# Kernel tuning notes

Measured on AMD Instinct MI355X. Metric: run time of the kernel, lower is better.

The kernel has to match this reference:

```python
import jax, jax.numpy as jnp
import numpy as np

INP_DIM, EMB_DIM, NUM_HEADS = 2048, 512, 2
LAMBDA_ATTN = 10.0
BS, L = 16, 1024


def _l2norm(x, axis=-1, eps=1e-12):
    # matches torch F.normalize: x / max(||x||, eps)
    n = jnp.sqrt(jnp.sum(x * x, axis=axis, keepdims=True))
    return x / jnp.maximum(n, eps)


def setup_inputs() -> dict:
    key = jax.random.key(0)
    k1, k2, kw, kb = jax.random.split(key, 4)
    img1 = jax.random.normal(k1, (BS, INP_DIM, L), dtype=jnp.float32)
    img2 = jax.random.normal(k2, (BS, INP_DIM, L), dtype=jnp.float32)
    # per-head query projection weights, stacked: (H, inp_dim, emb_dim)
    lim = 1.0 / np.sqrt(INP_DIM)
    W = jax.random.uniform(kw, (NUM_HEADS, INP_DIM, EMB_DIM), jnp.float32, -lim, lim)
    b = jax.random.uniform(kb, (NUM_HEADS, EMB_DIM), jnp.float32, -lim, lim)
    return {"img1": img1, "img2": img2, "W": W, "b": b}


def reference(img1, img2, W, b):
    # img1, img2: (bs, inp_dim, L) -> (bs, L, inp_dim)
    x1 = jnp.swapaxes(img1, 1, 2)
    x2 = jnp.swapaxes(img2, 1, 2)
    # per-head query projections: (H, bs, L, emb)
    q1 = jnp.einsum('bld,hde->hble', x1, W) + b[:, None, None, :]
    q2 = jnp.einsum('bld,hde->hble', x2, W) + b[:, None, None, :]
    # cosine relevance (attn_normalized=True): (H, bs, L, L)
    n1 = _l2norm(q1)
    n2 = _l2norm(q2)
    rel = jnp.einsum('hble,hbme->hblm', n1, n2) * LAMBDA_ATTN
    row_attn = jax.nn.softmax(rel, axis=3)  # softmax over img2 positions (dim=2 in torch)
    col_attn = jax.nn.softmax(rel, axis=2)  # softmax over img1 positions (dim=1 in torch)
    sim12 = row_attn.sum(axis=2)  # (H, bs, L) -> weight on img2 positions
    sim21 = col_attn.sum(axis=3)  # (H, bs, L) -> weight on img1 positions
    sim12 = sim12 / (sim12.sum(axis=-1, keepdims=True) + 1e-8)
    sim21 = sim21 / (sim21.sum(axis=-1, keepdims=True) + 1e-8)
    # torch module returns lists sim_in_img1 (=sim21) and sim_in_img2 (=sim12);
    # stack them: (2, H, bs, L)
    return jnp.stack([sim21, sim12], axis=0)
```

## Files before the change

kernel.cpp:

```cpp
#include <hip/hip_runtime.h>
#include <cstdint>
#include <cstddef>

#define INP 2048
#define EMB 512
#define NHEAD 2
#define BSZ 16
#define SEQ 1024
#define LAMBDA 10.0f

typedef __attribute__((ext_vector_type(8))) short bf16x8;
typedef __attribute__((ext_vector_type(16))) float f32x16;

__device__ __forceinline__ short f2bf(float x) {
    union { float f; unsigned u; } v; v.f = x;
    unsigned r = v.u + 0x7fffu + ((v.u >> 16) & 1u);
    return (short)(r >> 16);
}
__device__ __forceinline__ float bf2f(short h) {
    union { unsigned u; float f; } v; v.u = ((unsigned)(unsigned short)h) << 16;
    return v.f;
}
__device__ __forceinline__ void g2lds16(const void* g, void* l) {
    __builtin_amdgcn_global_load_lds(
        (const __attribute__((address_space(1))) unsigned int*)g,
        (__attribute__((address_space(3))) unsigned int*)l, 16, 0, 0);
}

__global__ __launch_bounds__(256) void zero_kernel(float* __restrict__ p, int n) {
    int i = blockIdx.x * 256 + threadIdx.x;
    if (i < n) p[i] = 0.f;
}

__global__ __launch_bounds__(256) void conv_t(const float* __restrict__ src,
                                              short* __restrict__ hi, int L) {
    const int l0 = blockIdx.x * 64;
    const int d0 = blockIdx.y * 32;
    const float* s = src + (size_t)blockIdx.z * INP * L;

    __shared__ float tl[32][65];
    const int t  = threadIdx.x;
    const int dr = t >> 3;
    const int f4 = (t & 7) * 4;

    float4 v0 = *(const float4*)&s[(size_t)(d0 + dr) * L + l0 + f4];
    float4 v1 = *(const float4*)&s[(size_t)(d0 + dr) * L + l0 + f4 + 32];
    tl[dr][f4 + 0] = v0.x; tl[dr][f4 + 1] = v0.y; tl[dr][f4 + 2] = v0.z; tl[dr][f4 + 3] = v0.w;
    tl[dr][f4 + 32] = v1.x; tl[dr][f4 + 33] = v1.y; tl[dr][f4 + 34] = v1.z; tl[dr][f4 + 35] = v1.w;
    __syncthreads();

    const int kgl = t >> 6;
    const int l   = t & 63;
    bf16x8 hv8;
#pragma unroll
    for (int q = 0; q < 8; q++) hv8[q] = f2bf(tl[kgl * 8 + q][l]);
    const size_t slot = (size_t)blockIdx.z * (INP / 8) * L
                      + (size_t)(blockIdx.y * 4 + kgl) * L + l0 + l;
    *(bf16x8*)&hi[slot * 8] = hv8;
}

__global__ __launch_bounds__(512, 2) void proj_gemm(
    const short* __restrict__ iT, const short* __restrict__ Wt,
    const float* __restrict__ bias, float* __restrict__ Q) {
    const int bid = blockIdx.x;
    const int xcd = bid & 7;
    const int s   = bid >> 3;
    const int g   = s >> 2;
    const int v   = s & 3;
    const int h   = v >> 1;
    const int nh  = v & 1;
    const int gg  = xcd * 16 + g;
    const int slab  = gg >> 2;
    const int mtile = gg & 3;
    const int mb = mtile * 256;
    const int nb = nh * 256;
    const int im = slab >> 4;
    const int b  = slab & 15;
    const int z  = (im * 2 + h) * 16 + b;

    const short* __restrict__ Ag = iT + (size_t)slab * (INP / 8) * SEQ * 8;
    const short* __restrict__ Bg = Wt + (size_t)h * (INP / 8) * EMB * 8;

    __shared__ short sL[4][16384];

    const int tid  = threadIdx.x;
    const int lane = tid & 63;
    const int wid  = tid >> 6;
    const int wm   = (wid >> 2) * 128;
    const int wn   = (wid & 3) * 64;
    const int fm   = lane & 31;
    const int khl  = lane >> 5;

    const int sgp = wid >> 2;
    const int srq = wid & 3;

    float bj[2];
#pragma unroll
    for (int j = 0; j < 2; j++) bj[j] = bias[h * EMB + nb + wn + j * 32 + fm];
    asm volatile("s_waitcnt vmcnt(0)" ::: "memory");

#define STAGE(tt) { \
    const int k8_ = (tt) * 4; \
    short* bA_ = &sL[(tt) & 3][0]; \
    short* bB_ = &sL[(tt) & 3][8192]; \
    g2lds16(Ag + ((size_t)(k8_ + sgp) * SEQ + mb + srq * 64 + lane) * 8, \
            bA_ + (sgp * 256 + srq * 64) * 8); \
    g2lds16(Ag + ((size_t)(k8_ + sgp + 2) * SEQ + mb + srq * 64 + lane) * 8, \
            bA_ + ((sgp + 2) * 256 + srq * 64) * 8); \
    g2lds16(Bg + ((size_t)(k8_ + sgp) * EMB + nb + srq * 64 + lane) * 8, \
            bB_ + (sgp * 256 + srq * 64) * 8); \
    g2lds16(Bg + ((size_t)(k8_ + sgp + 2) * EMB + nb + srq * 64 + lane) * 8, \
            bB_ + ((sgp + 2) * 256 + srq * 64) * 8); \
}

    f32x16 acc[4][2];
#pragma unroll
    for (int i = 0; i < 4; i++)
#pragma unroll
        for (int j = 0; j < 2; j++)
#pragma unroll
            for (int r = 0; r < 16; r++) acc[i][j][r] = 0.f;

    STAGE(0);
    STAGE(1);
    asm volatile("s_waitcnt vmcnt(4)" ::: "memory");
    __builtin_amdgcn_s_barrier();

    for (int t = 0; t < 64; t++) {
        if (t < 62) STAGE(t + 2);

        const short* bA = &sL[t & 3][0];
        const short* bB = &sL[t & 3][8192];
        bf16x8 af[4][2], bf[2][2];
#pragma unroll
        for (int ks = 0; ks < 2; ks++) {
            const int pl = (ks * 2 + khl) * 256;
#pragma unroll
            for (int i = 0; i < 4; i++)
                af[i][ks] = *(const bf16x8*)&bA[(pl + wm + i * 32 + fm) * 8];
#pragma unroll
            for (int j = 0; j < 2; j++)
                bf[j][ks] = *(const bf16x8*)&bB[(pl + wn + j * 32 + fm) * 8];
        }
        __builtin_amdgcn_s_setprio(1);
#pragma unroll
        for (int ks = 0; ks < 2; ks++)
#pragma unroll
            for (int i = 0; i < 4; i++)
#pragma unroll
                for (int j = 0; j < 2; j++)
                    acc[i][j] = __builtin_amdgcn_mfma_f32_32x32x16_bf16(af[i][ks], bf[j][ks], acc[i][j], 0, 0, 0);
        __builtin_amdgcn_s_setprio(0);

        if (t < 62)       asm volatile("s_waitcnt vmcnt(4)" ::: "memory");
        else if (t == 62) asm volatile("s_waitcnt vmcnt(0)" ::: "memory");
        if (t < 63) __builtin_amdgcn_s_barrier();
    }
#undef STAGE

    float* __restrict__ Qz = Q + (size_t)z * SEQ * EMB;
#pragma unroll
    for (int i = 0; i < 4; i++)
#pragma unroll
        for (int r = 0; r < 16; r++) {
            const int row = mb + wm + i * 32 + (r & 3) + 8 * (r >> 2) + khl * 4;
#pragma unroll
            for (int j = 0; j < 2; j++)
                Qz[(size_t)row * EMB + nb + wn + j * 32 + fm] = acc[i][j][r] + bj[j];
        }
}

__global__ __launch_bounds__(256) void norm_split(const float* __restrict__ Q,
                                                  short* __restrict__ Qhi) {
    const int z  = blockIdx.y;
    const int r0 = blockIdx.x * 4;
    const int t  = threadIdx.x;
    const int w    = t >> 6;
    const int lane = t & 63;
    const float* p = Q + ((size_t)z * SEQ + r0 + w) * EMB;

    float4 a = *(const float4*)&p[lane * 8];
    float4 b = *(const float4*)&p[lane * 8 + 4];
    float sq = a.x * a.x + a.y * a.y + a.z * a.z + a.w * a.w
             + b.x * b.x + b.y * b.y + b.z * b.z + b.w * b.w;
#pragma unroll
    for (int o = 32; o > 0; o >>= 1) sq += __shfl_xor(sq, o);
    float scale = 1.f / fmaxf(sqrtf(sq), 1e-12f);
    if (z < NHEAD * BSZ) scale *= LAMBDA;

    float v[8] = {a.x * scale, a.y * scale, a.z * scale, a.w * scale,
                  b.x * scale, b.y * scale, b.z * scale, b.w * scale};
    bf16x8 hv8;
#pragma unroll
    for (int q = 0; q < 8; q++) hv8[q] = f2bf(v[q]);
    __shared__ short shi[64 * 4 * 8];
    *(bf16x8*)&shi[(lane * 4 + w) * 8] = hv8;
    __syncthreads();

    const int kg = t >> 2, rl = t & 3;
    const size_t dst = ((size_t)z * (EMB / 8) + kg) * SEQ + r0 + rl;
    *(bf16x8*)&Qhi[dst * 8] = *(const bf16x8*)&shi[t * 8];
}

__global__ __launch_bounds__(256) void attn_mfma(
    const short* __restrict__ Qhi,
    short* __restrict__ E, float* __restrict__ Zr, float* __restrict__ Zc) {
    const int bid = blockIdx.x;
    const int xcd = bid & 7;
    const int s   = bid >> 3;
    const int hb  = xcd * 4 + (s >> 6);
    const int t   = s & 63;
    const int lt  = t & 7;
    const int mt  = t >> 3;
    const int l0 = lt * 128;
    const int m0 = mt * 128;

    const short* __restrict__ Ah = Qhi + (size_t)hb * SEQ * EMB;
    const short* __restrict__ Bh = Qhi + (size_t)(NHEAD * BSZ + hb) * SEQ * EMB;

    __shared__ short sA[4096], sB[4096];
    __shared__ float redR[128], redC[128];

    const int tid  = threadIdx.x;
    const int lane = tid & 63;
    const int wid  = tid >> 6;
    const int wm = (wid & 1) * 64;
    const int wn = (wid >> 1) * 64;
    const int fm = lane & 31;
    const int khl = lane >> 5;

    const short* gB = (wid & 2) ? Bh : Ah;
    short* lB = (wid & 2) ? sB : sA;
    const int rb = (wid & 2) ? m0 : l0;
    const int gb = (wid & 1) * 2;

    f32x16 acc[2][2];
#pragma unroll
    for (int i = 0; i < 2; i++)
#pragma unroll
        for (int j = 0; j < 2; j++)
#pragma unroll
            for (int r = 0; r < 16; r++) acc[i][j][r] = 0.f;

    for (int k0 = 0; k0 < EMB; k0 += 32) {
        const int k08 = k0 >> 3;
        __syncthreads();
#pragma unroll
        for (int v = 0; v < 4; v++) {
            const int g = gb + (v >> 1), hh = v & 1;
            g2lds16(gB + ((size_t)(k08 + g) * SEQ + rb + hh * 64 + lane) * 8,
                    lB + (g * 128 + hh * 64) * 8);
        }
        __syncthreads();

        bf16x8 afh[2][2], bfh[2][2];
#pragma unroll
        for (int i = 0; i < 2; i++)
#pragma unroll
            for (int ks = 0; ks < 2; ks++) {
                const int ra = ((ks * 2 + khl) * 128 + wm + i * 32 + fm) * 8;
                afh[i][ks] = *(const bf16x8*)&sA[ra];
                const int rbi = ((ks * 2 + khl) * 128 + wn + i * 32 + fm) * 8;
                bfh[i][ks] = *(const bf16x8*)&sB[rbi];
            }
#pragma unroll
        for (int ks = 0; ks < 2; ks++)
#pragma unroll
            for (int i = 0; i < 2; i++)
#pragma unroll
                for (int j = 0; j < 2; j++)
                    acc[i][j] = __builtin_amdgcn_mfma_f32_32x32x16_bf16(afh[i][ks], bfh[j][ks], acc[i][j], 0, 0, 0);
    }

    if (tid < 128) { redR[tid] = 0.f; redC[tid] = 0.f; }
    __syncthreads();

    short* __restrict__ Ez = E + (size_t)hb * SEQ * SEQ;
    const int rhalf = khl * 4;
    float cj0 = 0.f, cj1 = 0.f;
#pragma unroll
    for (int i = 0; i < 2; i++)
#pragma unroll
        for (int r = 0; r < 16; r++) {
            const int row = wm + i * 32 + (r & 3) + 8 * (r >> 2) + rhalf;
            const short e0s = f2bf(expf(acc[i][0][r]));
            const short e1s = f2bf(expf(acc[i][1][r]));
            const float e0v = bf2f(e0s);
            const float e1v = bf2f(e1s);
            Ez[(size_t)(l0 + row) * SEQ + m0 + wn + fm]      = e0s;
            Ez[(size_t)(l0 + row) * SEQ + m0 + wn + 32 + fm] = e1s;
            float rv = e0v + e1v;
#pragma unroll
            for (int o = 16; o > 0; o >>= 1) rv += __shfl_xor(rv, o);
            if ((lane & 31) == 0) atomicAdd(&redR[row], rv);
            cj0 += e0v; cj1 += e1v;
        }
    cj0 += __shfl_xor(cj0, 32);
    cj1 += __shfl_xor(cj1, 32);
    if (lane < 32) {
        atomicAdd(&redC[wn + fm], cj0);
        atomicAdd(&redC[wn + 32 + fm], cj1);
    }
    __syncthreads();

    if (tid < 128) {
        atomicAdd(&Zr[hb * SEQ + l0 + tid], redR[tid]);
        atomicAdd(&Zc[hb * SEQ + m0 + tid], redC[tid]);
    }
}

__global__ __launch_bounds__(256) void reduce_pass(
    const short* __restrict__ E, const float* __restrict__ Zr,
    const float* __restrict__ Zc, float* __restrict__ S21, float* __restrict__ S12) {
    const int lblk = blockIdx.x;
    const int hb   = blockIdx.y;
    const int tid  = threadIdx.x;
    const int lane = tid & 63;
    const int wid  = tid >> 6;
    const short* __restrict__ Ez = E + (size_t)hb * SEQ * SEQ;

    __shared__ float colred[SEQ];
    for (int i = tid; i < SEQ; i += 256) colred[i] = 0.f;
    __syncthreads();

    float izc[2][8];
#pragma unroll
    for (int it = 0; it < 2; it++)
#pragma unroll
        for (int q = 0; q < 8; q++)
            izc[it][q] = 1.f / Zc[hb * SEQ + it * 512 + lane * 8 + q];

    float colacc[2][8];
#pragma unroll
    for (int it = 0; it < 2; it++)
#pragma unroll
        for (int q = 0; q < 8; q++) colacc[it][q] = 0.f;

    for (int rr = 0; rr < 32; rr++) {
        const int row = lblk * 128 + wid * 32 + rr;
        const float izr = 1.f / Zr[hb * SEQ + row];
        float rowsum = 0.f;
#pragma unroll
        for (int it = 0; it < 2; it++) {
            bf16x8 ev = *(const bf16x8*)&Ez[(size_t)row * SEQ + it * 512 + lane * 8];
#pragma unroll
            for (int q = 0; q < 8; q++) {
                const float e = bf2f(ev[q]);
                rowsum += e * izc[it][q];
                colacc[it][q] += e * izr;
            }
        }
#pragma unroll
        for (int o = 32; o > 0; o >>= 1) rowsum += __shfl_down(rowsum, o);
        if (lane == 0) S21[hb * SEQ + row] = rowsum;
    }
#pragma unroll
    for (int it = 0; it < 2; it++)
#pragma unroll
        for (int q = 0; q < 8; q++)
            atomicAdd(&colred[it * 512 + lane * 8 + q], colacc[it][q]);
    __syncthreads();
    for (int i = tid; i < SEQ; i += 256) atomicAdd(&S12[hb * SEQ + i], colred[i]);
}

__global__ __launch_bounds__(256) void fin_kernel(
    const float* __restrict__ S21, const float* __restrict__ S12,
    float* __restrict__ out) {
    const int z  = blockIdx.x;
    const int w  = z / (NHEAD * BSZ);
    const int hb = z % (NHEAD * BSZ);
    const float* __restrict__ src = (w == 0 ? S21 : S12) + (size_t)hb * SEQ;
    const int t = threadIdx.x;

    float s = 0.f;
    for (int i = t; i < SEQ; i += 256) s += src[i];
#pragma unroll
    for (int o = 32; o > 0; o >>= 1) s += __shfl_down(s, o);
    __shared__ float red[4];
    if ((t & 63) == 0) red[t >> 6] = s;
    __syncthreads();
    const float total = red[0] + red[1] + red[2] + red[3];
    const float inv = 1.f / (total + 1e-8f);
    for (int i = t; i < SEQ; i += 256)
        out[(size_t)z * SEQ + i] = src[i] * inv;
}

extern "C" void kernel_launch(void* const* d_in, const int* in_sizes, int n_in,
                              void* d_out, int out_size, void* d_ws, size_t ws_size,
                              hipStream_t stream) {
    const float* img1 = (const float*)d_in[0];
    const float* img2 = (const float*)d_in[1];
    const float* W    = (const float*)d_in[2];
    const float* bias = (const float*)d_in[3];
    float* out = (float*)d_out;

    const size_t QN  = (size_t)2 * NHEAD * BSZ * SEQ * EMB;
    const size_t WN  = (size_t)NHEAD * EMB * INP;
    const size_t CNF = (size_t)32 * SEQ * INP;

    short* Qhi = (short*)d_ws;
    short* Wth = Qhi + QN;
    short* iTh = Wth + WN;
    float* Q   = (float*)(iTh + CNF);
    short* E   = (short*)Q;
    float* Zr  = Q + QN;
    float* Zc  = Zr + (size_t)NHEAD * BSZ * SEQ;
    float* S21 = Zc + (size_t)NHEAD * BSZ * SEQ;
    float* S12 = S21 + (size_t)NHEAD * BSZ * SEQ;

    zero_kernel<<<dim3(512), dim3(256), 0, stream>>>(Zr, 4 * NHEAD * BSZ * SEQ);

    conv_t<<<dim3(EMB / 64, INP / 32, NHEAD), dim3(256), 0, stream>>>(W, Wth, EMB);

    conv_t<<<dim3(SEQ / 64, INP / 32, 16), dim3(256), 0, stream>>>(img1, iTh, SEQ);
    conv_t<<<dim3(SEQ / 64, INP / 32, 16), dim3(256), 0, stream>>>(
        img2, iTh + (size_t)16 * (INP / 8) * SEQ * 8, SEQ);

    proj_gemm<<<dim3(512), dim3(512), 0, stream>>>(iTh, Wth, bias, Q);

    norm_split<<<dim3(SEQ / 4, 2 * NHEAD * BSZ), dim3(256), 0, stream>>>(Q, Qhi);

    attn_mfma<<<dim3(2048), dim3(256), 0, stream>>>(Qhi, E, Zr, Zc);

    reduce_pass<<<dim3(8, NHEAD * BSZ), dim3(256), 0, stream>>>(E, Zr, Zc, S21, S12);

    fin_kernel<<<dim3(2 * NHEAD * BSZ), dim3(256), 0, stream>>>(S21, S12, out);
    (void)in_sizes; (void)n_in; (void)out_size; (void)ws_size;
}
```

Before: 555.8 us.

## Switch projection and attention GEMMs to FP8 MFMA with register double-buffering

```diff
diff --git a/kernel.cpp b/kernel.cpp
--- a/kernel.cpp
+++ b/kernel.cpp
@@ -26,6 +26,40 @@
         (const __attribute__((address_space(1))) unsigned int*)g,
         (__attribute__((address_space(3))) unsigned int*)l, 16, 0, 0);
 }
+template <bool HI>
+__device__ __forceinline__ int pk8(float a, float b, int old) {
+    return __builtin_amdgcn_cvt_pk_fp8_f32(a, b, old, HI);
+}
+__device__ __forceinline__ void pack8f8(const float* v, unsigned* lo, unsigned* hi) {
+    int l = pk8<false>(v[0], v[1], 0); l = pk8<true>(v[2], v[3], l);
+    int h = pk8<false>(v[4], v[5], 0); h = pk8<true>(v[6], v[7], h);
+    *lo = (unsigned)l; *hi = (unsigned)h;
+}
+
+#define VM2() asm volatile("s_waitcnt vmcnt(2)" ::: "memory")
+#define VM0() asm volatile("s_waitcnt vmcnt(0)" ::: "memory")
+
+#define MFMAS(AO, BO) do { \
+    __builtin_amdgcn_s_setprio(1); \
+    _Pragma("unroll") for (int ks_ = 0; ks_ < 2; ks_++) \
+    _Pragma("unroll") for (int i_ = 0; i_ < 4; i_++) \
+    _Pragma("unroll") for (int j_ = 0; j_ < 2; j_++) \
+        acc[i_][j_] = __builtin_amdgcn_mfma_f32_32x32x16_fp8_fp8( \
+            AO[i_][ks_], BO[j_][ks_], acc[i_][j_], 0, 0, 0); \
+    __builtin_amdgcn_s_setprio(0); \
+} while (0)
+
+#define READF(AO, BO, sl) do { \
+    const char* bA_ = &sL[(sl)][0]; \
+    const char* bB_ = &sL[(sl)][8192]; \
+    _Pragma("unroll") for (int ks_ = 0; ks_ < 2; ks_++) { \
+        const int pl_ = (ks_ * 2 + khl) * 256; \
+        _Pragma("unroll") for (int i_ = 0; i_ < 4; i_++) \
+            AO[i_][ks_] = *(const long*)&bA_[(pl_ + wm + i_ * 32 + fm) * 8]; \
+        _Pragma("unroll") for (int j_ = 0; j_ < 2; j_++) \
+            BO[j_][ks_] = *(const long*)&bB_[(pl_ + wn + j_ * 32 + fm) * 8]; \
+    } \
+} while (0)
 
 __global__ __launch_bounds__(256) void zero_kernel(float* __restrict__ p, int n) {
     int i = blockIdx.x * 256 + threadIdx.x;
@@ -33,7 +67,7 @@
 }
 
 __global__ __launch_bounds__(256) void conv_t(const float* __restrict__ src,
-                                              short* __restrict__ hi, int L) {
+                                              char* __restrict__ out, int L) {
     const int l0 = blockIdx.x * 64;
     const int d0 = blockIdx.y * 32;
     const float* s = src + (size_t)blockIdx.z * INP * L;
@@ -51,16 +85,19 @@
 
     const int kgl = t >> 6;
     const int l   = t & 63;
-    bf16x8 hv8;
-#pragma unroll
-    for (int q = 0; q < 8; q++) hv8[q] = f2bf(tl[kgl * 8 + q][l]);
+    float v[8];
+#pragma unroll
+    for (int q = 0; q < 8; q++) v[q] = tl[kgl * 8 + q][l];
+    uint2 w;
+    pack8f8(v, &w.x, &w.y);
+
     const size_t slot = (size_t)blockIdx.z * (INP / 8) * L
                       + (size_t)(blockIdx.y * 4 + kgl) * L + l0 + l;
-    *(bf16x8*)&hi[slot * 8] = hv8;
+    *(uint2*)&out[slot * 8] = w;
 }
 
 __global__ __launch_bounds__(512, 2) void proj_gemm(
-    const short* __restrict__ iT, const short* __restrict__ Wt,
+    const char* __restrict__ iT, const char* __restrict__ Wt,
     const float* __restrict__ bias, float* __restrict__ Q) {
     const int bid = blockIdx.x;
     const int xcd = bid & 7;
@@ -78,10 +115,10 @@
     const int b  = slab & 15;
     const int z  = (im * 2 + h) * 16 + b;
 
-    const short* __restrict__ Ag = iT + (size_t)slab * (INP / 8) * SEQ * 8;
-    const short* __restrict__ Bg = Wt + (size_t)h * (INP / 8) * EMB * 8;
-
-    __shared__ short sL[4][16384];
+    const char* __restrict__ Ag = iT + (size_t)slab * INP * SEQ;
+    const char* __restrict__ Bg = Wt + (size_t)h * INP * EMB;
+
+    __shared__ char sL[4][16384];
 
     const int tid  = threadIdx.x;
     const int lane = tid & 63;
@@ -91,27 +128,18 @@
     const int fm   = lane & 31;
     const int khl  = lane >> 5;
 
-    const int sgp = wid >> 2;
-    const int srq = wid & 3;
+#define P_STAGE(tt) do { \
+    const int k8_ = (tt) * 4 + (wid >> 1); \
+    const int ro_ = (wid & 1) * 128 + lane * 2; \
+    char* d_ = &sL[(tt) & 3][(wid >> 1) * 2048 + (wid & 1) * 1024 + lane * 16]; \
+    g2lds16(Ag + ((size_t)k8_ * SEQ + mb + ro_) * 8, d_); \
+    g2lds16(Bg + ((size_t)k8_ * EMB + nb + ro_) * 8, d_ + 8192); \
+} while (0)
 
     float bj[2];
 #pragma unroll
     for (int j = 0; j < 2; j++) bj[j] = bias[h * EMB + nb + wn + j * 32 + fm];
-    asm volatile("s_waitcnt vmcnt(0)" ::: "memory");
-
-#define STAGE(tt) { \
-    const int k8_ = (tt) * 4; \
-    short* bA_ = &sL[(tt) & 3][0]; \
-    short* bB_ = &sL[(tt) & 3][8192]; \
-    g2lds16(Ag + ((size_t)(k8_ + sgp) * SEQ + mb + srq * 64 + lane) * 8, \
-            bA_ + (sgp * 256 + srq * 64) * 8); \
-    g2lds16(Ag + ((size_t)(k8_ + sgp + 2) * SEQ + mb + srq * 64 + lane) * 8, \
-            bA_ + ((sgp + 2) * 256 + srq * 64) * 8); \
-    g2lds16(Bg + ((size_t)(k8_ + sgp) * EMB + nb + srq * 64 + lane) * 8, \
-            bB_ + (sgp * 256 + srq * 64) * 8); \
-    g2lds16(Bg + ((size_t)(k8_ + sgp + 2) * EMB + nb + srq * 64 + lane) * 8, \
-            bB_ + ((sgp + 2) * 256 + srq * 64) * 8); \
-}
+    VM0();
 
     f32x16 acc[4][2];
 #pragma unroll
@@ -121,42 +149,28 @@
 #pragma unroll
             for (int r = 0; r < 16; r++) acc[i][j][r] = 0.f;
 
-    STAGE(0);
-    STAGE(1);
-    asm volatile("s_waitcnt vmcnt(4)" ::: "memory");
+    long a0[4][2], b0[2][2], a1[4][2], b1[2][2];
+
+    P_STAGE(0); P_STAGE(1); P_STAGE(2);
+    VM2();
     __builtin_amdgcn_s_barrier();
-
-    for (int t = 0; t < 64; t++) {
-        if (t < 62) STAGE(t + 2);
-
-        const short* bA = &sL[t & 3][0];
-        const short* bB = &sL[t & 3][8192];
-        bf16x8 af[4][2], bf[2][2];
-#pragma unroll
-        for (int ks = 0; ks < 2; ks++) {
-            const int pl = (ks * 2 + khl) * 256;
-#pragma unroll
-            for (int i = 0; i < 4; i++)
-                af[i][ks] = *(const bf16x8*)&bA[(pl + wm + i * 32 + fm) * 8];
-#pragma unroll
-            for (int j = 0; j < 2; j++)
-                bf[j][ks] = *(const bf16x8*)&bB[(pl + wn + j * 32 + fm) * 8];
-        }
-        __builtin_amdgcn_s_setprio(1);
-#pragma unroll
-        for (int ks = 0; ks < 2; ks++)
-#pragma unroll
-            for (int i = 0; i < 4; i++)
-#pragma unroll
-                for (int j = 0; j < 2; j++)
-                    acc[i][j] = __builtin_amdgcn_mfma_f32_32x32x16_bf16(af[i][ks], bf[j][ks], acc[i][j], 0, 0, 0);
-        __builtin_amdgcn_s_setprio(0);
-
-        if (t < 62)       asm volatile("s_waitcnt vmcnt(4)" ::: "memory");
-        else if (t == 62) asm volatile("s_waitcnt vmcnt(0)" ::: "memory");
-        if (t < 63) __builtin_amdgcn_s_barrier();
-    }
-#undef STAGE
+    READF(a0, b0, 0);
+
+    for (int t = 0; t < 64; t += 2) {
+        if (t + 3 < 64) P_STAGE(t + 3);
+        READF(a1, b1, (t + 1) & 3);
+        MFMAS(a0, b0);
+        if (t + 3 < 64) VM2();
+        __builtin_amdgcn_s_barrier();
+        const int u = t + 1;
+        if (u + 3 < 64) P_STAGE(u + 3);
+        if (u + 1 < 64) READF(a0, b0, (u + 1) & 3);
+        MFMAS(a1, b1);
+        if (u + 3 < 64) VM2();
+        else if (u == 61) VM0();
+        if (u + 1 < 64) __builtin_amdgcn_s_barrier();
+    }
+#undef P_STAGE
 
     float* __restrict__ Qz = Q + (size_t)z * SEQ * EMB;
 #pragma unroll
@@ -171,7 +185,7 @@
 }
 
 __global__ __launch_bounds__(256) void norm_split(const float* __restrict__ Q,
-                                                  short* __restrict__ Qhi) {
+                                                  char* __restrict__ Qf8) {
     const int z  = blockIdx.y;
     const int r0 = blockIdx.x * 4;
     const int t  = threadIdx.x;
@@ -190,99 +204,95 @@
 
     float v[8] = {a.x * scale, a.y * scale, a.z * scale, a.w * scale,
                   b.x * scale, b.y * scale, b.z * scale, b.w * scale};
-    bf16x8 hv8;
-#pragma unroll
-    for (int q = 0; q < 8; q++) hv8[q] = f2bf(v[q]);
-    __shared__ short shi[64 * 4 * 8];
-    *(bf16x8*)&shi[(lane * 4 + w) * 8] = hv8;
+    uint2 o2;
+    pack8f8(v, &o2.x, &o2.y);
+
+    __shared__ unsigned sh[64 * 4 * 2];
+    sh[(lane * 4 + w) * 2]     = o2.x;
+    sh[(lane * 4 + w) * 2 + 1] = o2.y;
     __syncthreads();
 
     const int kg = t >> 2, rl = t & 3;
     const size_t dst = ((size_t)z * (EMB / 8) + kg) * SEQ + r0 + rl;
-    *(bf16x8*)&Qhi[dst * 8] = *(const bf16x8*)&shi[t * 8];
-}
-
-__global__ __launch_bounds__(256) void attn_mfma(
-    const short* __restrict__ Qhi,
+    uint2 w2; w2.x = sh[t * 2]; w2.y = sh[t * 2 + 1];
+    *(uint2*)&Qf8[dst * 8] = w2;
+}
+
+__global__ __launch_bounds__(512, 2) void attn_mfma(
+    const char* __restrict__ Qf8,
     short* __restrict__ E, float* __restrict__ Zr, float* __restrict__ Zc) {
     const int bid = blockIdx.x;
     const int xcd = bid & 7;
     const int s   = bid >> 3;
-    const int hb  = xcd * 4 + (s >> 6);
-    const int t   = s & 63;
-    const int lt  = t & 7;
-    const int mt  = t >> 3;
-    const int l0 = lt * 128;
-    const int m0 = mt * 128;
-
-    const short* __restrict__ Ah = Qhi + (size_t)hb * SEQ * EMB;
-    const short* __restrict__ Bh = Qhi + (size_t)(NHEAD * BSZ + hb) * SEQ * EMB;
-
-    __shared__ short sA[4096], sB[4096];
-    __shared__ float redR[128], redC[128];
+    const int hb  = xcd * 8 + (s >> 4);
+    const int t4  = s & 15;
+    const int l0  = (t4 >> 2) * 256;
+    const int m0  = (t4 & 3) * 256;
+
+    const char* __restrict__ Ag = Qf8 + (size_t)hb * EMB * SEQ;
+    const char* __restrict__ Bg = Qf8 + (size_t)(NHEAD * BSZ + hb) * EMB * SEQ;
+
+    __shared__ char sL[4][16384];
+    __shared__ float redR[256], redC[256];
 
     const int tid  = threadIdx.x;
     const int lane = tid & 63;
     const int wid  = tid >> 6;
-    const int wm = (wid & 1) * 64;
-    const int wn = (wid >> 1) * 64;
-    const int fm = lane & 31;
-    const int khl = lane >> 5;
-
-    const short* gB = (wid & 2) ? Bh : Ah;
-    short* lB = (wid & 2) ? sB : sA;
-    const int rb = (wid & 2) ? m0 : l0;
-    const int gb = (wid & 1) * 2;
-
-    f32x16 acc[2][2];
-#pragma unroll
-    for (int i = 0; i < 2; i++)
+    const int wm   = (wid >> 2) * 128;
+    const int wn   = (wid & 3) * 64;
+    const int fm   = lane & 31;
+    const int khl  = lane >> 5;
+
+#define A_STAGE(tt) do { \
+    const int k8_ = (tt) * 4 + (wid >> 1); \
+    const int ro_ = (wid & 1) * 128 + lane * 2; \
+    char* d_ = &sL[(tt) & 3][(wid >> 1) * 2048 + (wid & 1) * 1024 + lane * 16]; \
+    g2lds16(Ag + ((size_t)k8_ * SEQ + l0 + ro_) * 8, d_); \
+    g2lds16(Bg + ((size_t)k8_ * SEQ + m0 + ro_) * 8, d_ + 8192); \
+} while (0)
+
+    f32x16 acc[4][2];
+#pragma unroll
+    for (int i = 0; i < 4; i++)
 #pragma unroll
         for (int j = 0; j < 2; j++)
 #pragma unroll
             for (int r = 0; r < 16; r++) acc[i][j][r] = 0.f;
 
-    for (int k0 = 0; k0 < EMB; k0 += 32) {
-        const int k08 = k0 >> 3;
-        __syncthreads();
-#pragma unroll
-        for (int v = 0; v < 4; v++) {
-            const int g = gb + (v >> 1), hh = v & 1;
-            g2lds16(gB + ((size_t)(k08 + g) * SEQ + rb + hh * 64 + lane) * 8,
-                    lB + (g * 128 + hh * 64) * 8);
-        }
-        __syncthreads();
-
-        bf16x8 afh[2][2], bfh[2][2];
-#pragma unroll
-        for (int i = 0; i < 2; i++)
-#pragma unroll
-            for (int ks = 0; ks < 2; ks++) {
-                const int ra = ((ks * 2 + khl) * 128 + wm + i * 32 + fm) * 8;
-                afh[i][ks] = *(const bf16x8*)&sA[ra];
-                const int rbi = ((ks * 2 + khl) * 128 + wn + i * 32 + fm) * 8;
-                bfh[i][ks] = *(const bf16x8*)&sB[rbi];
-            }
-#pragma unroll
-        for (int ks = 0; ks < 2; ks++)
-#pragma unroll
-            for (int i = 0; i < 2; i++)
-#pragma unroll
-                for (int j = 0; j < 2; j++)
-                    acc[i][j] = __builtin_amdgcn_mfma_f32_32x32x16_bf16(afh[i][ks], bfh[j][ks], acc[i][j], 0, 0, 0);
-    }
-
-    if (tid < 128) { redR[tid] = 0.f; redC[tid] = 0.f; }
+    long a0[4][2], b0[2][2], a1[4][2], b1[2][2];
+
+    A_STAGE(0); A_STAGE(1); A_STAGE(2);
+    VM2();
+    __builtin_amdgcn_s_barrier();
+    READF(a0, b0, 0);
+
+    for (int t = 0; t < 16; t += 2) {
+        if (t + 3 < 16) A_STAGE(t + 3);
+        READF(a1, b1, (t + 1) & 3);
+        MFMAS(a0, b0);
+        if (t + 3 < 16) VM2();
+        __builtin_amdgcn_s_barrier();
+        const int u = t + 1;
+        if (u + 3 < 16) A_STAGE(u + 3);
+        if (u + 1 < 16) READF(a0, b0, (u + 1) & 3);
+        MFMAS(a1, b1);
+        if (u + 3 < 16) VM2();
+        else if (u == 13) VM0();
+        if (u + 1 < 16) __builtin_amdgcn_s_barrier();
+    }
+#undef A_STAGE
+
+    if (tid < 256) { redR[tid] = 0.f; redC[tid] = 0.f; }
     __syncthreads();
 
     short* __restrict__ Ez = E + (size_t)hb * SEQ * SEQ;
-    const int rhalf = khl * 4;
     float cj0 = 0.f, cj1 = 0.f;
 #pragma unroll
-    for (int i = 0; i < 2; i++)
+    for (int i = 0; i < 4; i++) {
+        float ci0 = 0.f, ci1 = 0.f;
 #pragma unroll
         for (int r = 0; r < 16; r++) {
-            const int row = wm + i * 32 + (r & 3) + 8 * (r >> 2) + rhalf;
+            const int row = wm + i * 32 + (r & 3) + 8 * (r >> 2) + khl * 4;
             const short e0s = f2bf(expf(acc[i][0][r]));
             const short e1s = f2bf(expf(acc[i][1][r]));
             const float e0v = bf2f(e0s);
@@ -293,8 +303,10 @@
 #pragma unroll
             for (int o = 16; o > 0; o >>= 1) rv += __shfl_xor(rv, o);
             if ((lane & 31) == 0) atomicAdd(&redR[row], rv);
-            cj0 += e0v; cj1 += e1v;
+            ci0 += e0v; ci1 += e1v;
         }
+        cj0 += ci0; cj1 += ci1;
+    }
     cj0 += __shfl_xor(cj0, 32);
     cj1 += __shfl_xor(cj1, 32);
     if (lane < 32) {
@@ -303,7 +315,7 @@
     }
     __syncthreads();
 
-    if (tid < 128) {
+    if (tid < 256) {
         atomicAdd(&Zr[hb * SEQ + l0 + tid], redR[tid]);
         atomicAdd(&Zc[hb * SEQ + m0 + tid], redC[tid]);
     }
@@ -398,29 +410,29 @@
     const size_t WN  = (size_t)NHEAD * EMB * INP;
     const size_t CNF = (size_t)32 * SEQ * INP;
 
-    short* Qhi = (short*)d_ws;
-    short* Wth = Qhi + QN;
-    short* iTh = Wth + WN;
-    float* Q   = (float*)(iTh + CNF);
-    short* E   = (short*)Q;
-    float* Zr  = Q + QN;
+    char* Qf8 = (char*)d_ws;
+    char* Wf8 = Qf8 + QN;
+    char* iT8 = Wf8 + WN;
+    float* Q  = (float*)(iT8 + CNF);
+    short* E  = (short*)Q;
+    float* Zr = Q + QN;
     float* Zc  = Zr + (size_t)NHEAD * BSZ * SEQ;
     float* S21 = Zc + (size_t)NHEAD * BSZ * SEQ;
     float* S12 = S21 + (size_t)NHEAD * BSZ * SEQ;
 
     zero_kernel<<<dim3(512), dim3(256), 0, stream>>>(Zr, 4 * NHEAD * BSZ * SEQ);
 
-    conv_t<<<dim3(EMB / 64, INP / 32, NHEAD), dim3(256), 0, stream>>>(W, Wth, EMB);
-
-    conv_t<<<dim3(SEQ / 64, INP / 32, 16), dim3(256), 0, stream>>>(img1, iTh, SEQ);
+    conv_t<<<dim3(EMB / 64, INP / 32, NHEAD), dim3(256), 0, stream>>>(W, Wf8, EMB);
+
+    conv_t<<<dim3(SEQ / 64, INP / 32, 16), dim3(256), 0, stream>>>(img1, iT8, SEQ);
     conv_t<<<dim3(SEQ / 64, INP / 32, 16), dim3(256), 0, stream>>>(
-        img2, iTh + (size_t)16 * (INP / 8) * SEQ * 8, SEQ);
-
-    proj_gemm<<<dim3(512), dim3(512), 0, stream>>>(iTh, Wth, bias, Q);
-
-    norm_split<<<dim3(SEQ / 4, 2 * NHEAD * BSZ), dim3(256), 0, stream>>>(Q, Qhi);
-
-    attn_mfma<<<dim3(2048), dim3(256), 0, stream>>>(Qhi, E, Zr, Zc);
+        img2, iT8 + (size_t)16 * INP * SEQ, SEQ);
+
+    proj_gemm<<<dim3(512), dim3(512), 0, stream>>>(iT8, Wf8, bias, Q);
+
+    norm_split<<<dim3(SEQ / 4, 2 * NHEAD * BSZ), dim3(256), 0, stream>>>(Q, Qf8);
+
+    attn_mfma<<<dim3(1024), dim3(512), 0, stream>>>(Qf8, E, Zr, Zc);
 
     reduce_pass<<<dim3(8, NHEAD * BSZ), dim3(256), 0, stream>>>(E, Zr, Zc, S21, S12);
 
```

After: 583.2 us. +4.9%, slower.
